# Kernel tuning notes

Measured on AMD Instinct MI355X. Metric: run time of the kernel, lower is better.

## Reference

```python
import jax, jax.numpy as jnp
import numpy as np


def setup_inputs() -> dict:
    key = jax.random.key(0)
    ks = jax.random.split(key, 6)
    B, T, S, E, D = 8, 128, 512, 512, 512  # batch, trg_len, src_len, enc_dim, trg_dim
    W_SCALE = 0.03  # small init to keep tanh unsaturated
    return {
        "hidden": jax.random.normal(ks[0], (B, T, D), jnp.float32),
        "encoder_outputs": jax.random.normal(ks[1], (B, S, E), jnp.float32),
        "encoder_mask": jnp.ones((B, S), jnp.float32),
        "W_attn": jax.random.normal(ks[2], (D, E + D), jnp.float32) * W_SCALE,
        "b_attn": jnp.zeros((D,), jnp.float32),
        "W_v": jax.random.normal(ks[3], (1, D), jnp.float32) * W_SCALE,
        "b_v": jnp.zeros((1,), jnp.float32),
        "W_out": jax.random.normal(ks[4], (D, E + D), jnp.float32) * W_SCALE,
    }


def masked_softmax(x, m, axis=-1):
    # faithful to repo: x*m, stable exp, e*m, normalize with eps
    x = x * m
    e_x = jnp.exp(x - jnp.max(x, axis=axis, keepdims=True))
    e_x = e_x * m
    return e_x / (jnp.sum(e_x, axis=axis, keepdims=True) + 1e-6)


def reference(hidden, encoder_outputs, encoder_mask, W_attn, b_attn, W_v, b_v, W_out):
    B, T, D = hidden.shape
    S = encoder_outputs.shape[1]
    # concat order in get_energy is (hidden_i, encoder_outputs), so split W_attn
    W_h = W_attn[:, :D]   # (D_out, trg_dim)
    W_e = W_attn[:, D:]   # (D_out, enc_dim)
    # Linear(concat) == h@W_h^T + e@W_e^T + b; vectorized over all (t, s) pairs
    hp = jnp.einsum('btd,kd->btk', hidden, W_h)            # (B,T,K)
    ep = jnp.einsum('bse,ke->bsk', encoder_outputs, W_e)   # (B,S,K)
    feat = jnp.tanh(hp[:, :, None, :] + ep[:, None, :, :] + b_attn)  # (B,T,S,K)
    energies = jnp.einsum('btsk,k->bts', feat, W_v[0]) + b_v[0]      # (B,T,S)
    # forward: energies * mask, then masked softmax
    m = encoder_mask[:, None, :]  # (B,1,S)
    energies = energies * m
    attn_weights = masked_softmax(energies, m, axis=-1)    # (B,T,S)
    weighted_context = jnp.einsum('bts,bse->bte', attn_weights, encoder_outputs)
    h_cat = jnp.concatenate([weighted_context, hidden], axis=-1)  # (B,T,E+D)
    h_tilde = jnp.tanh(jnp.einsum('btc,dc->btd', h_cat, W_out))   # (B,T,D)
    return h_tilde, weighted_context, attn_weights
```

## Files before the change

kernel.cpp:

```cpp
#include <hip/hip_runtime.h>
#include <hip/hip_bf16.h>
#include <math.h>

typedef unsigned short u16;
typedef unsigned int u32;
typedef __bf16 bf16x8 __attribute__((ext_vector_type(8)));
typedef float f32x4 __attribute__((ext_vector_type(4)));

#define OUT_WC   524288LL
#define OUT_ATTN 1048576LL
#define C2 2.8853900817779268f
#define LOG2E 1.4426950408889634f
#define LAS 40

__device__ inline u16 f2b(float f) {
    return (u16)((__float_as_uint(f) + 0x8000u) >> 16);
}
__device__ inline float b2f(u16 v) { return __uint_as_float(((u32)v) << 16); }
__device__ inline u32 pkcvt(float x, float y) {
    __hip_bfloat162 h = __float22bfloat162_rn(make_float2(x, y));
    return *(u32*)&h;
}
__device__ inline float tanh_fast(float x) {
    return 1.f - 2.f * __builtin_amdgcn_rcpf(__builtin_amdgcn_exp2f(C2 * x) + 1.f);
}

__global__ __launch_bounds__(256) void tobf(
    const float* __restrict__ enc, const float* __restrict__ hidden,
    const float* __restrict__ Wattn, const float* __restrict__ Wout,
    u16* __restrict__ dst)
{
    long long i = ((long long)blockIdx.x * 256 + threadIdx.x) * 8;
    const float* src; long long off;
    if (i < 2097152)      { src = enc;    off = i; }
    else if (i < 2621440) { src = hidden; off = i - 2097152; }
    else if (i < 3145728) { src = Wattn;  off = i - 2621440; }
    else                  { src = Wout;   off = i - 3145728; }
    float4 v0 = *(const float4*)(src + off);
    float4 v1 = *(const float4*)(src + off + 4);
    *(uint4*)(dst + i) = make_uint4(pkcvt(v0.x, v0.y), pkcvt(v0.z, v0.w),
                                    pkcvt(v1.x, v1.y), pkcvt(v1.z, v1.w));
}

__global__ __launch_bounds__(256) void proj(
    const u16* __restrict__ hidden_bf, const u16* __restrict__ enc_bf,
    const u16* __restrict__ Wattn_bf, const float* __restrict__ battn,
    const u16* __restrict__ Wout_bf,
    float* __restrict__ hp, u16* __restrict__ ept, float* __restrict__ hh)
{
    __shared__ u16 lA[64 * LAS];
    __shared__ u16 lB[64 * LAS];
    const int tid = threadIdx.x;
    const int wvi = tid >> 6, ln = tid & 63;
    const int wm = wvi >> 1, wn = wvi & 1;
    const int l16 = ln & 15, quad = ln >> 4;
    const int blk = blockIdx.x;
    int bx, by, zz = 0, lda, ldb, mode;
    const u16 *A, *B;
    if (blk < 512) {
        mode = 0;
        zz = blk >> 6; by = (blk >> 3) & 7; bx = blk & 7;
        A = Wattn_bf + 512; lda = 1024;
        B = enc_bf + (long long)zz * 262144; ldb = 512;
    } else if (blk < 640) {
        mode = 1;
        int i = blk - 512; by = i >> 3; bx = i & 7;
        A = hidden_bf; lda = 512;
        B = Wattn_bf; ldb = 1024;
    } else {
        mode = 2;
        int i = blk - 640; by = i >> 3; bx = i & 7;
        A = hidden_bf; lda = 512;
        B = Wout_bf + 512; ldb = 1024;
    }
    const int m0 = by * 64, n0 = bx * 64;
    const int srow = tid >> 2, skof = (tid & 3) * 8;
    const u16* Ap = A + (long long)(m0 + srow) * lda + skof;
    const u16* Bp = B + (long long)(n0 + srow) * ldb + skof;

    f32x4 acc00 = {0,0,0,0}, acc01 = {0,0,0,0}, acc10 = {0,0,0,0}, acc11 = {0,0,0,0};

    for (int k0 = 0; k0 < 512; k0 += 32) {
        uint4 av = *(const uint4*)(Ap + k0);
        uint4 bv = *(const uint4*)(Bp + k0);
        __syncthreads();
        *(uint4*)&lA[srow * LAS + skof] = av;
        *(uint4*)&lB[srow * LAS + skof] = bv;
        __syncthreads();
        bf16x8 a0 = *(const bf16x8*)&lA[(wm * 32      + l16) * LAS + quad * 8];
        bf16x8 a1 = *(const bf16x8*)&lA[(wm * 32 + 16 + l16) * LAS + quad * 8];
        bf16x8 b0 = *(const bf16x8*)&lB[(wn * 32      + l16) * LAS + quad * 8];
        bf16x8 b1 = *(const bf16x8*)&lB[(wn * 32 + 16 + l16) * LAS + quad * 8];
        acc00 = __builtin_amdgcn_mfma_f32_16x16x32_bf16(a0, b0, acc00, 0, 0, 0);
        acc01 = __builtin_amdgcn_mfma_f32_16x16x32_bf16(a0, b1, acc01, 0, 0, 0);
        acc10 = __builtin_amdgcn_mfma_f32_16x16x32_bf16(a1, b0, acc10, 0, 0, 0);
        acc11 = __builtin_amdgcn_mfma_f32_16x16x32_bf16(a1, b1, acc11, 0, 0, 0);
    }

    const f32x4* accs[4] = { &acc00, &acc01, &acc10, &acc11 };
    #pragma unroll
    for (int i = 0; i < 2; ++i) {
        #pragma unroll
        for (int j = 0; j < 2; ++j) {
            const f32x4& a = *accs[i * 2 + j];
            #pragma unroll
            for (int r = 0; r < 4; ++r) {
                int m = m0 + wm * 32 + i * 16 + quad * 4 + r;
                int n = n0 + wn * 32 + j * 16 + l16;
                float v = a[r];
                if (mode == 0)
                    ept[(long long)zz * 262144 + (long long)m * 512 + n] =
                        f2b(__builtin_amdgcn_exp2f(C2 * v));
                else if (mode == 1)
                    hp[(long long)m * 512 + n] = C2 * (v + battn[n]);
                else
                    hh[(long long)m * 512 + n] = v;
            }
        }
    }
}

__device__ inline float wred_sum(float v) {
    #pragma unroll
    for (int i = 32; i > 0; i >>= 1) v += __shfl_xor(v, i);
    return v;
}
__device__ inline float bred_sum8(float v, float* red, int tid) {
    v = wred_sum(v);
    __syncthreads();
    if ((tid & 63) == 0) red[tid >> 6] = v;
    __syncthreads();
    float s = 0.f;
    #pragma unroll
    for (int i = 0; i < 8; ++i) s += red[i];
    return s;
}
__device__ inline void bred2_max(float v0, float v1, float* red, int tid,
                                 float* o0, float* o1) {
    #pragma unroll
    for (int i = 32; i > 0; i >>= 1) {
        v0 = fmaxf(v0, __shfl_xor(v0, i));
        v1 = fmaxf(v1, __shfl_xor(v1, i));
    }
    __syncthreads();
    if ((tid & 63) == 0) { red[tid >> 6] = v0; red[8 + (tid >> 6)] = v1; }
    __syncthreads();
    float a0 = red[0], a1 = red[8];
    #pragma unroll
    for (int i = 1; i < 8; ++i) { a0 = fmaxf(a0, red[i]); a1 = fmaxf(a1, red[8 + i]); }
    *o0 = a0; *o1 = a1;
}
__device__ inline void bred2_sum(float v0, float v1, float* red, int tid,
                                 float* o0, float* o1) {
    #pragma unroll
    for (int i = 32; i > 0; i >>= 1) { v0 += __shfl_xor(v0, i); v1 += __shfl_xor(v1, i); }
    __syncthreads();
    if ((tid & 63) == 0) { red[tid >> 6] = v0; red[8 + (tid >> 6)] = v1; }
    __syncthreads();
    float a0 = 0.f, a1 = 0.f;
    #pragma unroll
    for (int i = 0; i < 8; ++i) { a0 += red[i]; a1 += red[8 + i]; }
    *o0 = a0; *o1 = a1;
}

__device__ inline void proc8(uint4 c, float4 hw, float* a0, float* a1) {
    u32 cc[4] = {c.x, c.y, c.z, c.w};
    #pragma unroll
    for (int i = 0; i < 4; ++i) {
        float xl = __uint_as_float(cc[i] << 16);
        float xh = __uint_as_float(cc[i] & 0xFFFF0000u);
        float rl0 = __builtin_amdgcn_rcpf(fmaf(hw.x, xl, 1.f));
        float rh0 = __builtin_amdgcn_rcpf(fmaf(hw.x, xh, 1.f));
        float rl1 = __builtin_amdgcn_rcpf(fmaf(hw.y, xl, 1.f));
        float rh1 = __builtin_amdgcn_rcpf(fmaf(hw.y, xh, 1.f));
        a0[2*i]   = fmaf(hw.z, rl0, a0[2*i]);
        a0[2*i+1] = fmaf(hw.z, rh0, a0[2*i+1]);
        a1[2*i]   = fmaf(hw.z, rl1, a1[2*i]);
        a1[2*i+1] = fmaf(hw.z, rh1, a1[2*i+1]);
    }
}

__global__ __launch_bounds__(512) void energies(
    const float* __restrict__ maskp, const float* __restrict__ hp,
    const u16* __restrict__ ept, const float* __restrict__ Wv,
    const float* __restrict__ bvp, const u16* __restrict__ enc_bf,
    float* __restrict__ attn, float* __restrict__ wc)
{
    __shared__ __align__(16) float4 hpw[512];
    __shared__ float pa[2][8][512];
    __shared__ __align__(16) float2 aL[512];
    __shared__ float red[16];
    const int tid = threadIdx.x;
    const int b = blockIdx.x >> 6;
    const int t0 = (blockIdx.x & 63) * 2;

    float w = Wv[tid];
    float h0 = hp[(long long)(b * 128 + t0) * 512 + tid];
    float h1 = hp[(long long)(b * 128 + t0 + 1) * 512 + tid];
    hpw[tid] = make_float4(__builtin_amdgcn_exp2f(h0), __builtin_amdgcn_exp2f(h1), w, 0.f);
    float sumWv = bred_sum8(w, red, tid);

    const int kg = tid >> 6, sl = tid & 63;
    const int s0 = sl * 8;
    const u16* eb = ept + (long long)b * 262144 + (kg * 64) * 512 + s0;
    const float4* hq = &hpw[kg * 64];

    float a0[8] = {0,0,0,0,0,0,0,0}, a1[8] = {0,0,0,0,0,0,0,0};
    uint4 c0 = *(const uint4*)(eb);
    uint4 c1 = *(const uint4*)(eb + 512);
    uint4 c2 = *(const uint4*)(eb + 1024);
    uint4 c3 = *(const uint4*)(eb + 1536);
    for (int kk = 0; kk < 60; kk += 4) {
        const u16* nb = eb + (kk + 4) * 512;
        uint4 n0 = *(const uint4*)(nb);
        uint4 n1 = *(const uint4*)(nb + 512);
        uint4 n2 = *(const uint4*)(nb + 1024);
        uint4 n3 = *(const uint4*)(nb + 1536);
        proc8(c0, hq[kk],     a0, a1);
        proc8(c1, hq[kk + 1], a0, a1);
        proc8(c2, hq[kk + 2], a0, a1);
        proc8(c3, hq[kk + 3], a0, a1);
        c0 = n0; c1 = n1; c2 = n2; c3 = n3;
    }
    proc8(c0, hq[60], a0, a1);
    proc8(c1, hq[61], a0, a1);
    proc8(c2, hq[62], a0, a1);
    proc8(c3, hq[63], a0, a1);

    *(float4*)&pa[0][kg][s0]     = make_float4(a0[0], a0[1], a0[2], a0[3]);
    *(float4*)&pa[0][kg][s0 + 4] = make_float4(a0[4], a0[5], a0[6], a0[7]);
    *(float4*)&pa[1][kg][s0]     = make_float4(a1[0], a1[1], a1[2], a1[3]);
    *(float4*)&pa[1][kg][s0 + 4] = make_float4(a1[4], a1[5], a1[6], a1[7]);
    __syncthreads();

    const int s = tid;
    float A0 = 0.f, A1 = 0.f;
    #pragma unroll
    for (int g = 0; g < 8; ++g) { A0 += pa[0][g][s]; A1 += pa[1][g][s]; }
    float mv = maskp[(long long)b * 512 + s];
    float bv0 = bvp[0];
    float r0 = (bv0 + sumWv - 2.f * A0) * mv; r0 *= mv;
    float r1 = (bv0 + sumWv - 2.f * A1) * mv; r1 *= mv;

    float mx0, mx1;
    bred2_max(r0, r1, red, tid, &mx0, &mx1);
    float ex0 = __builtin_amdgcn_exp2f((r0 - mx0) * LOG2E) * mv;
    float ex1 = __builtin_amdgcn_exp2f((r1 - mx1) * LOG2E) * mv;
    float sm0, sm1;
    bred2_sum(ex0, ex1, red, tid, &sm0, &sm1);
    float at0 = ex0 * (1.f / (sm0 + 1e-6f));
    float at1 = ex1 * (1.f / (sm1 + 1e-6f));
    attn[(long long)(b * 128 + t0) * 512 + s]     = at0;
    attn[(long long)(b * 128 + t0 + 1) * 512 + s] = at1;
    aL[s] = make_float2(at0, at1);
    __syncthreads();

    const u16* encb = enc_bf + (long long)b * 262144 + tid;
    const float4* aL4 = (const float4*)aL;
    float acc0 = 0.f, acc1 = 0.f;
    for (int ss = 0; ss < 512; ss += 8) {
        float ev[8];
        #pragma unroll
        for (int i = 0; i < 8; ++i) ev[i] = b2f(encb[(ss + i) * 512]);
        #pragma unroll
        for (int i = 0; i < 4; ++i) {
            float4 ap = aL4[(ss >> 1) + i];
            acc0 = fmaf(ap.x, ev[2*i],   acc0);
            acc1 = fmaf(ap.y, ev[2*i],   acc1);
            acc0 = fmaf(ap.z, ev[2*i+1], acc0);
            acc1 = fmaf(ap.w, ev[2*i+1], acc1);
        }
    }
    wc[(long long)(b * 128 + t0) * 512 + tid]     = acc0;
    wc[(long long)(b * 128 + t0 + 1) * 512 + tid] = acc1;
}

__global__ __launch_bounds__(256) void hout_k(
    const float* __restrict__ wc, const u16* __restrict__ Wout_bf,
    float* __restrict__ out)
{
    __shared__ u16 lA[32 * LAS];
    __shared__ u16 lB[64 * LAS];
    const int tid = threadIdx.x;
    const int wvi = tid >> 6, ln = tid & 63;
    const int l16 = ln & 15, quad = ln >> 4;
    const int msub = wvi & 1, npair = wvi >> 1;
    const int m0 = blockIdx.y * 32, n0 = blockIdx.x * 64;
    const int rowA = tid >> 3, kofA = (tid & 7) * 4;
    const int rowB = tid >> 2, kofB = (tid & 3) * 8;
    f32x4 acc0 = {0,0,0,0}, acc1 = {0,0,0,0};

    for (int k0 = 0; k0 < 512; k0 += 32) {
        float4 av = *(const float4*)(wc + (long long)(m0 + rowA) * 512 + k0 + kofA);
        uint4 bv = *(const uint4*)(Wout_bf + (long long)(n0 + rowB) * 1024 + k0 + kofB);
        __syncthreads();
        *(uint2*)&lA[rowA * LAS + kofA] = make_uint2(pkcvt(av.x, av.y), pkcvt(av.z, av.w));
        int kk = kofB ^ (((rowB >> 3) & 3) << 3);
        *(uint4*)&lB[rowB * LAS + kk] = bv;
        __syncthreads();
        bf16x8 a = *(const bf16x8*)&lA[(msub * 16 + l16) * LAS + quad * 8];
        int nr0 = npair * 32 + l16, nr1 = nr0 + 16;
        bf16x8 b0 = *(const bf16x8*)&lB[nr0 * LAS + (quad * 8 ^ (((nr0 >> 3) & 3) << 3))];
        bf16x8 b1 = *(const bf16x8*)&lB[nr1 * LAS + (quad * 8 ^ (((nr1 >> 3) & 3) << 3))];
        acc0 = __builtin_amdgcn_mfma_f32_16x16x32_bf16(a, b0, acc0, 0, 0, 0);
        acc1 = __builtin_amdgcn_mfma_f32_16x16x32_bf16(a, b1, acc1, 0, 0, 0);
    }
    #pragma unroll
    for (int j = 0; j < 2; ++j) {
        const f32x4& a = j ? acc1 : acc0;
        #pragma unroll
        for (int r = 0; r < 4; ++r) {
            int m = m0 + msub * 16 + quad * 4 + r;
            int n = n0 + npair * 32 + j * 16 + l16;
            long long idx = (long long)m * 512 + n;
            out[idx] = tanh_fast(a[r] + out[idx]);
        }
    }
}

extern "C" void kernel_launch(void* const* d_in, const int* in_sizes, int n_in,
                              void* d_out, int out_size, void* d_ws, size_t ws_size,
                              hipStream_t stream)
{
    const float* hidden = (const float*)d_in[0];
    const float* enc    = (const float*)d_in[1];
    const float* mask   = (const float*)d_in[2];
    const float* Wattn  = (const float*)d_in[3];
    const float* battn  = (const float*)d_in[4];
    const float* Wv     = (const float*)d_in[5];
    const float* bvp    = (const float*)d_in[6];
    const float* Wout   = (const float*)d_in[7];
    float* out = (float*)d_out;

    float* hp  = (float*)d_ws;
    u16*   ept = (u16*)((char*)d_ws + (2 << 20));
    u16*   bfp = (u16*)((char*)d_ws + (6 << 20));
    u16* enc_bf    = bfp;
    u16* hidden_bf = bfp + 2097152;
    u16* Wattn_bf  = bfp + 2621440;
    u16* Wout_bf   = bfp + 3145728;

    tobf<<<1792, 256, 0, stream>>>(enc, hidden, Wattn, Wout, bfp);
    proj<<<768, 256, 0, stream>>>(hidden_bf, enc_bf, Wattn_bf, battn, Wout_bf,
                                  hp, ept, out );
    energies<<<512, 512, 0, stream>>>(mask, hp, ept, Wv, bvp, enc_bf,
                                      out + OUT_ATTN, out + OUT_WC);
    hout_k<<<dim3(8, 32, 1), 256, 0, stream>>>(out + OUT_WC, Wout_bf, out);
}
```

Before: 148.3 us.

## Double energies block to 1024 threads with split-K and vectorized context reduction

The energies kernel now runs 1024 threads per block. The K dimension of the tanh-energy sum is split across 16 wave groups of 32 rows each instead of 8 of 64, and each half of the block handles one of the two target rows in the softmax. The weighted-context pass is restructured: each thread loads 8 bf16 encoder values per row with vector loads over a 32-row S slice, then partial sums are reduced through shared memory, replacing the scalar strided per-column loads. This adds shared-memory traffic and extra barriers, and the larger block may limit occupancy.

```diff
diff --git a/kernel.cpp b/kernel.cpp
--- a/kernel.cpp
+++ b/kernel.cpp
@@ -125,42 +125,10 @@
     for (int i = 32; i > 0; i >>= 1) v += __shfl_xor(v, i);
     return v;
 }
-__device__ inline float bred_sum8(float v, float* red, int tid) {
-    v = wred_sum(v);
-    __syncthreads();
-    if ((tid & 63) == 0) red[tid >> 6] = v;
-    __syncthreads();
-    float s = 0.f;
-    #pragma unroll
-    for (int i = 0; i < 8; ++i) s += red[i];
-    return s;
-}
-__device__ inline void bred2_max(float v0, float v1, float* red, int tid,
-                                 float* o0, float* o1) {
-    #pragma unroll
-    for (int i = 32; i > 0; i >>= 1) {
-        v0 = fmaxf(v0, __shfl_xor(v0, i));
-        v1 = fmaxf(v1, __shfl_xor(v1, i));
-    }
-    __syncthreads();
-    if ((tid & 63) == 0) { red[tid >> 6] = v0; red[8 + (tid >> 6)] = v1; }
-    __syncthreads();
-    float a0 = red[0], a1 = red[8];
-    #pragma unroll
-    for (int i = 1; i < 8; ++i) { a0 = fmaxf(a0, red[i]); a1 = fmaxf(a1, red[8 + i]); }
-    *o0 = a0; *o1 = a1;
-}
-__device__ inline void bred2_sum(float v0, float v1, float* red, int tid,
-                                 float* o0, float* o1) {
-    #pragma unroll
-    for (int i = 32; i > 0; i >>= 1) { v0 += __shfl_xor(v0, i); v1 += __shfl_xor(v1, i); }
-    __syncthreads();
-    if ((tid & 63) == 0) { red[tid >> 6] = v0; red[8 + (tid >> 6)] = v1; }
-    __syncthreads();
-    float a0 = 0.f, a1 = 0.f;
-    #pragma unroll
-    for (int i = 0; i < 8; ++i) { a0 += red[i]; a1 += red[8 + i]; }
-    *o0 = a0; *o1 = a1;
+__device__ inline float wred_max(float v) {
+    #pragma unroll
+    for (int i = 32; i > 0; i >>= 1) v = fmaxf(v, __shfl_xor(v, i));
+    return v;
 }
 
 __device__ inline void proc8(uint4 c, float4 hw, float* a0, float* a1) {
@@ -180,37 +148,47 @@
     }
 }
 
-__global__ __launch_bounds__(512) void energies(
+__global__ __launch_bounds__(1024, 8) void energies(
     const float* __restrict__ maskp, const float* __restrict__ hp,
     const u16* __restrict__ ept, const float* __restrict__ Wv,
     const float* __restrict__ bvp, const u16* __restrict__ enc_bf,
     float* __restrict__ attn, float* __restrict__ wc)
 {
     __shared__ __align__(16) float4 hpw[512];
-    __shared__ float pa[2][8][512];
-    __shared__ __align__(16) float2 aL[512];
+    __shared__ float pa[2][16][512];
+    __shared__ __align__(8) float aL[512][2];
     __shared__ float red[16];
     const int tid = threadIdx.x;
-    const int b = blockIdx.x >> 6;
+    const int b  = blockIdx.x >> 6;
     const int t0 = (blockIdx.x & 63) * 2;
-
-    float w = Wv[tid];
-    float h0 = hp[(long long)(b * 128 + t0) * 512 + tid];
-    float h1 = hp[(long long)(b * 128 + t0 + 1) * 512 + tid];
-    hpw[tid] = make_float4(__builtin_amdgcn_exp2f(h0), __builtin_amdgcn_exp2f(h1), w, 0.f);
-    float sumWv = bred_sum8(w, red, tid);
+    const int th = tid >> 9;
+    const int k5 = tid & 511;
+
+    float hv = hp[(long long)(b * 128 + t0 + th) * 512 + k5];
+    float eh = __builtin_amdgcn_exp2f(hv);
+    float* hpwf = (float*)hpw;
+    hpwf[k5 * 4 + th] = eh;
+    float w = 0.f;
+    if (th == 0) { w = Wv[k5]; hpwf[k5 * 4 + 2] = w; }
+    float wsum = wred_sum(w);
+    __syncthreads();
+    if ((tid & 63) == 0) red[tid >> 6] = wsum;
+    __syncthreads();
+    float sumWv = 0.f;
+    #pragma unroll
+    for (int i = 0; i < 16; ++i) sumWv += red[i];
 
     const int kg = tid >> 6, sl = tid & 63;
     const int s0 = sl * 8;
-    const u16* eb = ept + (long long)b * 262144 + (kg * 64) * 512 + s0;
-    const float4* hq = &hpw[kg * 64];
+    const u16* eb = ept + (long long)b * 262144 + (kg * 32) * 512 + s0;
+    const float4* hq = &hpw[kg * 32];
 
     float a0[8] = {0,0,0,0,0,0,0,0}, a1[8] = {0,0,0,0,0,0,0,0};
     uint4 c0 = *(const uint4*)(eb);
     uint4 c1 = *(const uint4*)(eb + 512);
     uint4 c2 = *(const uint4*)(eb + 1024);
     uint4 c3 = *(const uint4*)(eb + 1536);
-    for (int kk = 0; kk < 60; kk += 4) {
+    for (int kk = 0; kk < 28; kk += 4) {
         const u16* nb = eb + (kk + 4) * 512;
         uint4 n0 = *(const uint4*)(nb);
         uint4 n1 = *(const uint4*)(nb + 512);
@@ -222,10 +200,10 @@
         proc8(c3, hq[kk + 3], a0, a1);
         c0 = n0; c1 = n1; c2 = n2; c3 = n3;
     }
-    proc8(c0, hq[60], a0, a1);
-    proc8(c1, hq[61], a0, a1);
-    proc8(c2, hq[62], a0, a1);
-    proc8(c3, hq[63], a0, a1);
+    proc8(c0, hq[28], a0, a1);
+    proc8(c1, hq[29], a0, a1);
+    proc8(c2, hq[30], a0, a1);
+    proc8(c3, hq[31], a0, a1);
 
     *(float4*)&pa[0][kg][s0]     = make_float4(a0[0], a0[1], a0[2], a0[3]);
     *(float4*)&pa[0][kg][s0 + 4] = make_float4(a0[4], a0[5], a0[6], a0[7]);
@@ -233,46 +211,61 @@
     *(float4*)&pa[1][kg][s0 + 4] = make_float4(a1[4], a1[5], a1[6], a1[7]);
     __syncthreads();
 
-    const int s = tid;
-    float A0 = 0.f, A1 = 0.f;
-    #pragma unroll
-    for (int g = 0; g < 8; ++g) { A0 += pa[0][g][s]; A1 += pa[1][g][s]; }
-    float mv = maskp[(long long)b * 512 + s];
+    float A = 0.f;
+    #pragma unroll
+    for (int g = 0; g < 16; ++g) A += pa[th][g][k5];
+    float mv = maskp[(long long)b * 512 + k5];
     float bv0 = bvp[0];
-    float r0 = (bv0 + sumWv - 2.f * A0) * mv; r0 *= mv;
-    float r1 = (bv0 + sumWv - 2.f * A1) * mv; r1 *= mv;
-
-    float mx0, mx1;
-    bred2_max(r0, r1, red, tid, &mx0, &mx1);
-    float ex0 = __builtin_amdgcn_exp2f((r0 - mx0) * LOG2E) * mv;
-    float ex1 = __builtin_amdgcn_exp2f((r1 - mx1) * LOG2E) * mv;
-    float sm0, sm1;
-    bred2_sum(ex0, ex1, red, tid, &sm0, &sm1);
-    float at0 = ex0 * (1.f / (sm0 + 1e-6f));
-    float at1 = ex1 * (1.f / (sm1 + 1e-6f));
-    attn[(long long)(b * 128 + t0) * 512 + s]     = at0;
-    attn[(long long)(b * 128 + t0 + 1) * 512 + s] = at1;
-    aL[s] = make_float2(at0, at1);
-    __syncthreads();
-
-    const u16* encb = enc_bf + (long long)b * 262144 + tid;
-    const float4* aL4 = (const float4*)aL;
-    float acc0 = 0.f, acc1 = 0.f;
-    for (int ss = 0; ss < 512; ss += 8) {
-        float ev[8];
-        #pragma unroll
-        for (int i = 0; i < 8; ++i) ev[i] = b2f(encb[(ss + i) * 512]);
+    float r = (bv0 + sumWv - 2.f * A) * mv; r *= mv;
+
+    float vmax = wred_max(r);
+    __syncthreads();
+    if ((tid & 63) == 0) red[tid >> 6] = vmax;
+    __syncthreads();
+    float mx = red[th * 8];
+    #pragma unroll
+    for (int i = 1; i < 8; ++i) mx = fmaxf(mx, red[th * 8 + i]);
+
+    float ex = __builtin_amdgcn_exp2f((r - mx) * LOG2E) * mv;
+    float vsum = wred_sum(ex);
+    __syncthreads();
+    if ((tid & 63) == 0) red[tid >> 6] = vsum;
+    __syncthreads();
+    float sm = 0.f;
+    #pragma unroll
+    for (int i = 0; i < 8; ++i) sm += red[th * 8 + i];
+    float at = ex * (1.f / (sm + 1e-6f));
+    attn[(long long)(b * 128 + t0 + th) * 512 + k5] = at;
+    aL[k5][th] = at;
+    __syncthreads();
+
+    const int eg = tid & 63, sg = tid >> 6;
+    const u16* encb = enc_bf + (long long)b * 262144 + (long long)(sg * 32) * 512 + eg * 8;
+    float acc0[8] = {0,0,0,0,0,0,0,0}, acc1[8] = {0,0,0,0,0,0,0,0};
+    for (int j = 0; j < 32; ++j) {
+        uint4 ev = *(const uint4*)(encb + j * 512);
+        float2 ap = *(const float2*)&aL[sg * 32 + j][0];
+        u32 cc[4] = {ev.x, ev.y, ev.z, ev.w};
         #pragma unroll
         for (int i = 0; i < 4; ++i) {
-            float4 ap = aL4[(ss >> 1) + i];
-            acc0 = fmaf(ap.x, ev[2*i],   acc0);
-            acc1 = fmaf(ap.y, ev[2*i],   acc1);
-            acc0 = fmaf(ap.z, ev[2*i+1], acc0);
-            acc1 = fmaf(ap.w, ev[2*i+1], acc1);
+            float el = __uint_as_float(cc[i] << 16);
+            float ehh = __uint_as_float(cc[i] & 0xFFFF0000u);
+            acc0[2*i]   = fmaf(ap.x, el,  acc0[2*i]);
+            acc0[2*i+1] = fmaf(ap.x, ehh, acc0[2*i+1]);
+            acc1[2*i]   = fmaf(ap.y, el,  acc1[2*i]);
+            acc1[2*i+1] = fmaf(ap.y, ehh, acc1[2*i+1]);
         }
     }
-    wc[(long long)(b * 128 + t0) * 512 + tid]     = acc0;
-    wc[(long long)(b * 128 + t0 + 1) * 512 + tid] = acc1;
+    *(float4*)&pa[0][sg][eg * 8]     = make_float4(acc0[0], acc0[1], acc0[2], acc0[3]);
+    *(float4*)&pa[0][sg][eg * 8 + 4] = make_float4(acc0[4], acc0[5], acc0[6], acc0[7]);
+    *(float4*)&pa[1][sg][eg * 8]     = make_float4(acc1[0], acc1[1], acc1[2], acc1[3]);
+    *(float4*)&pa[1][sg][eg * 8 + 4] = make_float4(acc1[4], acc1[5], acc1[6], acc1[7]);
+    __syncthreads();
+
+    float wcv = 0.f;
+    #pragma unroll
+    for (int g = 0; g < 16; ++g) wcv += pa[th][g][k5];
+    wc[(long long)(b * 128 + t0 + th) * 512 + k5] = wcv;
 }
 
 __global__ __launch_bounds__(256) void hout_k(
@@ -343,7 +336,7 @@
     tobf<<<1792, 256, 0, stream>>>(enc, hidden, Wattn, Wout, bfp);
     proj<<<768, 256, 0, stream>>>(hidden_bf, enc_bf, Wattn_bf, battn, Wout_bf,
                                   hp, ept, out );
-    energies<<<512, 512, 0, stream>>>(mask, hp, ept, Wv, bvp, enc_bf,
-                                      out + OUT_ATTN, out + OUT_WC);
+    energies<<<512, 1024, 0, stream>>>(mask, hp, ept, Wv, bvp, enc_bf,
+                                       out + OUT_ATTN, out + OUT_WC);
     hout_k<<<dim3(8, 32, 1), 256, 0, stream>>>(out + OUT_WC, Wout_bf, out);
 }
```

New measurement: 186.5 us. 25.8% more time.
